# Performance work log

Measured on AMD Instinct MI355X. Metric: run time of the kernel, lower is better.

The kernel has to match this reference:

```python
import jax, jax.numpy as jnp
import numpy as np

N = 4096          # in_features
M = 4096          # out_features
RANK = 64
FT = 16           # ft_rank (trainable LoRA)
RES = RANK - FT   # frozen low-rank residual
CB = 65536        # E8P: 16-bit codeword per group of 8 weights
CW = 8            # codeword width (E8 lattice dim)
Q_SCALE = 0.02
GLOBAL_SCALE = 1.0


def _hadamard(n):
    # Sylvester construction, normalized: H @ H.T = I (matches matmul_hadU/hadUt up to transpose; H is symmetric)
    H = np.array([[1.0]], dtype=np.float32)
    while H.shape[0] < n:
        H = np.block([[H, H], [H, -H]])
    return H / np.sqrt(np.float32(n))


def setup_inputs() -> dict:
    key = jax.random.key(0)
    ks = jax.random.split(key, 9)
    x = jax.random.normal(ks[0], (8192, N), jnp.float32)
    Q_idxs = jax.random.randint(ks[1], (M, N // CW), 0, CB, dtype=jnp.int32)
    grid = jax.random.normal(ks[2], (CB, CW), jnp.float32) * 0.5   # E8P codebook grid
    SU = jax.random.rademacher(ks[3], (N,), dtype=jnp.float32)     # random sign vectors (QuIP#)
    SV = jax.random.rademacher(ks[4], (M,), dtype=jnp.float32)
    L_ft = jax.random.normal(ks[5], (M, FT), jnp.float32) * 0.02
    R_ft = jax.random.normal(ks[6], (FT, N), jnp.float32) * 0.02
    L_res = jax.random.normal(ks[7], (M, RES), jnp.float32) * 0.02
    R_res = jax.random.normal(ks[8], (RES, N), jnp.float32) * 0.02
    had_left = jnp.asarray(_hadamard(N))
    had_right = jnp.asarray(_hadamard(M))
    return {"x": x, "SU": SU, "SV": SV, "grid": grid, "L_ft": L_ft, "R_ft": R_ft,
            "L_res": L_res, "R_res": R_res, "had_left": had_left,
            "had_right": had_right, "Q_idxs": Q_idxs}


def reference(x, SU, SV, grid, L_ft, R_ft, L_res, R_res, had_left, had_right, Q_idxs):
    shape = x.shape
    h = x.reshape(-1, N) * SU                 # x * SU
    h = h @ had_left                          # matmul_hadUt (Hadamard is symmetric orthogonal)
    # E8P codebook decode: gather 8-dim codewords -> full [M, N] weight, fused matmul
    W = grid[Q_idxs].reshape(M, N)            # [M, N//8, 8] -> [M, N]
    out = (h @ W.T) * Q_SCALE                 # Q.forward
    out = out + (h @ R_res.T) @ L_res.T       # frozen low-rank residual (rank - ft_rank)
    out = out + (h @ R_ft.T) @ L_ft.T         # trainable LoRA path
    out = (out @ had_right) * GLOBAL_SCALE    # matmul_hadU * global_scale
    out = out * SV
    return out.reshape(*shape[:-1], M)
```

## Files before the change

kernel.cpp:

```cpp
#include <hip/hip_runtime.h>
#include <hip/hip_bf16.h>
#include <stdint.h>


typedef __bf16 bf16;
typedef __bf16 bf16x8 __attribute__((ext_vector_type(8)));
typedef float f32x4 __attribute__((ext_vector_type(4)));

#define KE 4160
#define NN 4096
#define MM 4096
#define BB 8192

__global__ void prep_kernel(const float* __restrict__ Lft, const float* __restrict__ Rft,
                            const float* __restrict__ Lres, const float* __restrict__ Rres,
                            bf16* __restrict__ Rcat, bf16* __restrict__ Wq) {
  int tid = blockIdx.x * 256 + threadIdx.x;
  if (tid < 64 * 4096) {
    int r = tid >> 12, n = tid & 4095;
    float v = (r < 48) ? Rres[r * 4096 + n] : Rft[(r - 48) * 4096 + n];
    Rcat[tid] = (bf16)v;
  } else {
    int t2 = tid - 64 * 4096;
    int m = t2 >> 6, r = t2 & 63;
    float v = (r < 48) ? Lres[m * 48 + r] : Lft[m * 16 + (r - 48)];
    Wq[(size_t)m * KE + 4096 + r] = (bf16)v;
  }
}

__global__ void decode_kernel(const int* __restrict__ qidx, const float* __restrict__ grid,
                              bf16* __restrict__ Wq) {
  int tid = blockIdx.x * 256 + threadIdx.x;
  int m = tid >> 9, g = tid & 511;
  uint32_t idx = (uint32_t)qidx[tid];
  const float4* gp = (const float4*)(grid + (size_t)idx * 8);
  float4 w0 = gp[0], w1 = gp[1];
  bf16x8 o;
  o[0] = (bf16)(w0.x * 0.02f); o[1] = (bf16)(w0.y * 0.02f);
  o[2] = (bf16)(w0.z * 0.02f); o[3] = (bf16)(w0.w * 0.02f);
  o[4] = (bf16)(w1.x * 0.02f); o[5] = (bf16)(w1.y * 0.02f);
  o[6] = (bf16)(w1.z * 0.02f); o[7] = (bf16)(w1.w * 0.02f);
  *(bf16x8*)(Wq + (size_t)m * KE + g * 8) = o;
}

#define SK(i) ((i) + ((i) >> 5))

__global__ void fwht_pre_kernel(const float* __restrict__ src,
                                bf16* __restrict__ dst,
                                const float* __restrict__ SU) {
  __shared__ float buf[4224];
  const int row = blockIdx.x, t = threadIdx.x;
  const float4* sp = (const float4*)(src + (size_t)row * NN + t * 16);
  const float4* su = (const float4*)(SU + t * 16);
  float v[16];
#pragma unroll
  for (int q = 0; q < 4; ++q) {
    float4 a = sp[q], s = su[q];
    v[q * 4 + 0] = a.x * s.x; v[q * 4 + 1] = a.y * s.y;
    v[q * 4 + 2] = a.z * s.z; v[q * 4 + 3] = a.w * s.w;
  }
#pragma unroll
  for (int s = 1; s < 16; s <<= 1) {
#pragma unroll
    for (int i = 0; i < 16; ++i) {
      if (!(i & s)) { float a = v[i], b = v[i + s]; v[i] = a + b; v[i + s] = a - b; }
    }
  }
#pragma unroll
  for (int i = 0; i < 16; ++i) buf[SK(t * 16 + i)] = v[i];
  for (int s = 16; s < 4096; s <<= 1) {
    __syncthreads();
#pragma unroll
    for (int j = 0; j < 8; ++j) {
      int p = t + j * 256;
      int i = ((p & ~(s - 1)) << 1) | (p & (s - 1));
      float a = buf[SK(i)], b = buf[SK(i + s)];
      buf[SK(i)] = a + b; buf[SK(i + s)] = a - b;
    }
  }
  __syncthreads();
  bf16x8 o0, o1;
#pragma unroll
  for (int i = 0; i < 8; ++i) {
    o0[i] = (bf16)(buf[SK(t * 16 + i)] * 0.015625f);
    o1[i] = (bf16)(buf[SK(t * 16 + 8 + i)] * 0.015625f);
  }
  bf16* dp = dst + (size_t)row * KE + t * 16;
  *(bf16x8*)dp = o0;
  *(bf16x8*)(dp + 8) = o1;
}

__global__ void fwht_post_kernel(float* __restrict__ data, const float* __restrict__ SV) {
  __shared__ float buf[4224];
  const int row = blockIdx.x, t = threadIdx.x;
  float4* dp = (float4*)(data + (size_t)row * MM + t * 16);
  float v[16];
#pragma unroll
  for (int q = 0; q < 4; ++q) {
    float4 a = dp[q];
    v[q * 4 + 0] = a.x; v[q * 4 + 1] = a.y; v[q * 4 + 2] = a.z; v[q * 4 + 3] = a.w;
  }
#pragma unroll
  for (int s = 1; s < 16; s <<= 1) {
#pragma unroll
    for (int i = 0; i < 16; ++i) {
      if (!(i & s)) { float a = v[i], b = v[i + s]; v[i] = a + b; v[i + s] = a - b; }
    }
  }
#pragma unroll
  for (int i = 0; i < 16; ++i) buf[SK(t * 16 + i)] = v[i];
  for (int s = 16; s < 4096; s <<= 1) {
    __syncthreads();
#pragma unroll
    for (int j = 0; j < 8; ++j) {
      int p = t + j * 256;
      int i = ((p & ~(s - 1)) << 1) | (p & (s - 1));
      float a = buf[SK(i)], b = buf[SK(i + s)];
      buf[SK(i)] = a + b; buf[SK(i + s)] = a - b;
    }
  }
  __syncthreads();
  const float4* sv = (const float4*)(SV + t * 16);
#pragma unroll
  for (int q = 0; q < 4; ++q) {
    float4 s = sv[q];
    float4 o;
    o.x = buf[SK(t * 16 + q * 4 + 0)] * 0.015625f * s.x;
    o.y = buf[SK(t * 16 + q * 4 + 1)] * 0.015625f * s.y;
    o.z = buf[SK(t * 16 + q * 4 + 2)] * 0.015625f * s.z;
    o.w = buf[SK(t * 16 + q * 4 + 3)] * 0.015625f * s.w;
    dp[q] = o;
  }
}

__global__ void __launch_bounds__(256) tgemm_kernel(const bf16* __restrict__ A,
                                                    const bf16* __restrict__ Bm,
                                                    float* __restrict__ Tpart) {
  __shared__ bf16 lA[128 * 32];
  __shared__ bf16 lB[64 * 32];
  const int t = threadIdx.x, w = t >> 6, l = t & 63;
  const int bmBlk = blockIdx.x;
  const int split = blockIdx.y;
  const int wm = w >> 1, wn = w & 1;
  f32x4 acc[4][2] = {};
  const int arow = t >> 1, acol = (t & 1) * 16;
  const bf16* pa = A + (size_t)(bmBlk * 128 + arow) * KE + acol;
  const int brow = (t & 127) >> 1, bcol = acol;
  const bf16* pb = Bm + (size_t)brow * 4096 + bcol;
  const int fr = l & 15, fk = (l >> 4) * 8;
  for (int kt = 0; kt < 32; ++kt) {
    const int k0 = (split * 32 + kt) * 32;
    bf16x8 a0 = *(const bf16x8*)(pa + k0);
    bf16x8 a1 = *(const bf16x8*)(pa + k0 + 8);
    *(bf16x8*)&lA[arow * 32 + acol] = a0;
    *(bf16x8*)&lA[arow * 32 + acol + 8] = a1;
    if (t < 128) {
      bf16x8 b0 = *(const bf16x8*)(pb + k0);
      bf16x8 b1 = *(const bf16x8*)(pb + k0 + 8);
      *(bf16x8*)&lB[brow * 32 + bcol] = b0;
      *(bf16x8*)&lB[brow * 32 + bcol + 8] = b1;
    }
    __syncthreads();
    bf16x8 af[4], bfr[2];
#pragma unroll
    for (int i = 0; i < 4; ++i) af[i] = *(const bf16x8*)&lA[(wm * 64 + i * 16 + fr) * 32 + fk];
#pragma unroll
    for (int i = 0; i < 2; ++i) bfr[i] = *(const bf16x8*)&lB[(wn * 32 + i * 16 + fr) * 32 + fk];
#pragma unroll
    for (int mi = 0; mi < 4; ++mi)
#pragma unroll
      for (int ni = 0; ni < 2; ++ni)
        acc[mi][ni] = __builtin_amdgcn_mfma_f32_16x16x32_bf16(af[mi], bfr[ni], acc[mi][ni], 0, 0, 0);
    __syncthreads();
  }
  float* out = Tpart + (size_t)split * BB * 64;
  const int orow = bmBlk * 128 + wm * 64 + (l >> 4) * 4;
  const int ocol = wn * 32 + (l & 15);
#pragma unroll
  for (int mi = 0; mi < 4; ++mi)
#pragma unroll
    for (int ni = 0; ni < 2; ++ni)
#pragma unroll
      for (int r = 0; r < 4; ++r)
        out[(size_t)(orow + mi * 16 + r) * 64 + ocol + ni * 16] = acc[mi][ni][r];
}

__global__ void tconv_kernel(const float* __restrict__ Tpart, bf16* __restrict__ h) {
  int i = blockIdx.x * 256 + threadIdx.x;
  float s = Tpart[i] + Tpart[i + BB * 64] + Tpart[i + 2 * BB * 64] + Tpart[i + 3 * BB * 64];
  int row = i >> 6, c = i & 63;
  h[(size_t)row * KE + 4096 + c] = (bf16)s;
}


__device__ __forceinline__ void gload16(const void* g, void* l) {
  __builtin_amdgcn_global_load_lds(
      (const __attribute__((address_space(1))) void*)g,
      (__attribute__((address_space(3))) void*)l, 16, 0, 0);
}

__device__ __forceinline__ void bar() {
  asm volatile("" ::: "memory");
  __builtin_amdgcn_s_barrier();
  asm volatile("" ::: "memory");
}

__global__ void __launch_bounds__(512, 2) mgemm_kernel(const bf16* __restrict__ A,
                                                       const bf16* __restrict__ B,
                                                       float* __restrict__ C) {
  __shared__ alignas(16) char sA[65536];
  __shared__ alignas(16) char sB[65536];
  const int t = threadIdx.x;
  const int w = t >> 6, l = t & 63;
  const int wm = w >> 2, wn = w & 3;
  const int bid = blockIdx.x;
  const int swzb = (bid & 7) * 64 + (bid >> 3);
  const int bm = swzb >> 4, bn = swzb & 15;

  const int c0 = w * 2, c1 = w * 2 + 1;
  const int lb0 = c0 * 1024 + l * 16;
  const int lb1 = c1 * 1024 + l * 16;
  const int sb0 = lb0 ^ (((lb0 >> 7) & 3) << 4);
  const int sb1 = lb1 ^ (((lb1 >> 7) & 3) << 4);
  const char* gA0 = (const char*)(A + (size_t)(bm * 256 + (sb0 >> 6)) * KE) + (sb0 & 63);
  const char* gA1 = (const char*)(A + (size_t)(bm * 256 + (sb1 >> 6)) * KE) + (sb1 & 63);
  const char* gB0 = (const char*)(B + (size_t)(bn * 256 + (sb0 >> 6)) * KE) + (sb0 & 63);
  const char* gB1 = (const char*)(B + (size_t)(bn * 256 + (sb1 >> 6)) * KE) + (sb1 & 63);

  const int fr = l & 15, fkb = (l >> 4) * 16;
  int offA[8], offB[4];
#pragma unroll
  for (int mi = 0; mi < 8; ++mi) {
    int lb = (wm * 128 + mi * 16 + fr) * 64 + fkb;
    offA[mi] = lb ^ (((lb >> 7) & 3) << 4);
  }
#pragma unroll
  for (int ni = 0; ni < 4; ++ni) {
    int lb = (wn * 64 + ni * 16 + fr) * 64 + fkb;
    offB[ni] = lb ^ (((lb >> 7) & 3) << 4);
  }

  f32x4 acc[8][4] = {};

#pragma unroll
  for (int p = 0; p < 3; ++p) {
    gload16(gA0 + (size_t)p * 64, &sA[p * 16384 + c0 * 1024]);
    gload16(gA1 + (size_t)p * 64, &sA[p * 16384 + c1 * 1024]);
    gload16(gB0 + (size_t)p * 64, &sB[p * 16384 + c0 * 1024]);
    gload16(gB1 + (size_t)p * 64, &sB[p * 16384 + c1 * 1024]);
  }
  asm volatile("s_waitcnt vmcnt(8)" ::: "memory");
  __builtin_amdgcn_sched_barrier(0);
  bar();

  for (int i = 0; i < 130; ++i) {
    const int sbs = (i & 3) << 14;
    const int s3b = ((i + 3) & 3) << 14;
    const size_t ko = (size_t)(i + 3) << 6;
    if (i < 127) {
      gload16(gA0 + ko, &sA[s3b + c0 * 1024]);
      gload16(gA1 + ko, &sA[s3b + c1 * 1024]);
      gload16(gB0 + ko, &sB[s3b + c0 * 1024]);
      gload16(gB1 + ko, &sB[s3b + c1 * 1024]);
    }
    bf16x8 af[8], bv[4];
#pragma unroll
    for (int ni = 0; ni < 4; ++ni) bv[ni] = *(const bf16x8*)&sB[sbs + offB[ni]];
#pragma unroll
    for (int mi = 0; mi < 8; ++mi) af[mi] = *(const bf16x8*)&sA[sbs + offA[mi]];
    __builtin_amdgcn_s_setprio(1);
#pragma unroll
    for (int mi = 0; mi < 8; ++mi)
#pragma unroll
      for (int ni = 0; ni < 4; ++ni)
        acc[mi][ni] = __builtin_amdgcn_mfma_f32_16x16x32_bf16(af[mi], bv[ni], acc[mi][ni], 0, 0, 0);
    __builtin_amdgcn_s_setprio(0);
    if (i < 127) {
      asm volatile("s_waitcnt vmcnt(8)" ::: "memory");
    } else if (i == 127) {
      asm volatile("s_waitcnt vmcnt(4)" ::: "memory");
    } else if (i == 128) {
      asm volatile("s_waitcnt vmcnt(0)" ::: "memory");
    }
    __builtin_amdgcn_sched_barrier(0);
    bar();
  }

  const int orow = bm * 256 + wm * 128 + ((l >> 4) << 2);
  const int ocol = bn * 256 + wn * 64 + (l & 15);
#pragma unroll
  for (int mi = 0; mi < 8; ++mi)
#pragma unroll
    for (int ni = 0; ni < 4; ++ni)
#pragma unroll
      for (int r = 0; r < 4; ++r)
        C[(size_t)(orow + mi * 16 + r) * MM + ocol + ni * 16] = acc[mi][ni][r];
}

extern "C" void kernel_launch(void* const* d_in, const int* in_sizes, int n_in,
                              void* d_out, int out_size, void* d_ws, size_t ws_size,
                              hipStream_t stream) {
  const float* x    = (const float*)d_in[0];
  const float* SU   = (const float*)d_in[1];
  const float* SV   = (const float*)d_in[2];
  const float* grid = (const float*)d_in[3];
  const float* Lft  = (const float*)d_in[4];
  const float* Rft  = (const float*)d_in[5];
  const float* Lres = (const float*)d_in[6];
  const float* Rres = (const float*)d_in[7];
  const int*   qidx = (const int*)d_in[10];
  float* out = (float*)d_out;

  char* ws = (char*)d_ws;
  bf16*  h     = (bf16*)ws;
  bf16*  Wq    = (bf16*)(ws + 68157440);
  bf16*  Rcat  = (bf16*)(ws + 68157440 + 34078720);
  float* Tpart = (float*)(ws + 68157440 + 34078720 + 524288);

  prep_kernel<<<2048, 256, 0, stream>>>(Lft, Rft, Lres, Rres, Rcat, Wq);
  decode_kernel<<<8192, 256, 0, stream>>>(qidx, grid, Wq);
  fwht_pre_kernel<<<8192, 256, 0, stream>>>(x, h, SU);
  tgemm_kernel<<<dim3(64, 4), 256, 0, stream>>>(h, Rcat, Tpart);
  tconv_kernel<<<2048, 256, 0, stream>>>(Tpart, h);
  mgemm_kernel<<<512, 512, 0, stream>>>(h, Wq, out);
  fwht_post_kernel<<<8192, 256, 0, stream>>>(out, SV);
}
```

Baseline: 714.4 us.

## Interleave GEMM LDS reads, global loads and MFMA in half-tile phases; drop FWHT padding

The main GEMM loop is unrolled by two K-steps and split into four phases. Each phase reads half the A fragments, issues part of the next global-to-LDS loads, hits a barrier, then runs 16 MFMAs, so memory traffic and compute interleave more finely, in the style of a ping-pong schedule. This adds many more barriers per iteration and changes the vmcnt wait accounting, which could stall or race if the counts are wrong. The FWHT kernels also drop the shared-memory padding swizzle, which may bring back LDS bank conflicts on the butterfly strides.

```diff
diff --git a/kernel.cpp b/kernel.cpp
--- a/kernel.cpp
+++ b/kernel.cpp
@@ -43,12 +43,10 @@
   *(bf16x8*)(Wq + (size_t)m * KE + g * 8) = o;
 }
 
-#define SK(i) ((i) + ((i) >> 5))
-
 __global__ void fwht_pre_kernel(const float* __restrict__ src,
                                 bf16* __restrict__ dst,
                                 const float* __restrict__ SU) {
-  __shared__ float buf[4224];
+  __shared__ float buf[4096];
   const int row = blockIdx.x, t = threadIdx.x;
   const float4* sp = (const float4*)(src + (size_t)row * NN + t * 16);
   const float4* su = (const float4*)(SU + t * 16);
@@ -67,23 +65,23 @@
     }
   }
 #pragma unroll
-  for (int i = 0; i < 16; ++i) buf[SK(t * 16 + i)] = v[i];
+  for (int i = 0; i < 16; ++i) buf[t * 16 + i] = v[i];
   for (int s = 16; s < 4096; s <<= 1) {
     __syncthreads();
 #pragma unroll
     for (int j = 0; j < 8; ++j) {
       int p = t + j * 256;
       int i = ((p & ~(s - 1)) << 1) | (p & (s - 1));
-      float a = buf[SK(i)], b = buf[SK(i + s)];
-      buf[SK(i)] = a + b; buf[SK(i + s)] = a - b;
+      float a = buf[i], b = buf[i + s];
+      buf[i] = a + b; buf[i + s] = a - b;
     }
   }
   __syncthreads();
   bf16x8 o0, o1;
 #pragma unroll
   for (int i = 0; i < 8; ++i) {
-    o0[i] = (bf16)(buf[SK(t * 16 + i)] * 0.015625f);
-    o1[i] = (bf16)(buf[SK(t * 16 + 8 + i)] * 0.015625f);
+    o0[i] = (bf16)(buf[t * 16 + i] * 0.015625f);
+    o1[i] = (bf16)(buf[t * 16 + 8 + i] * 0.015625f);
   }
   bf16* dp = dst + (size_t)row * KE + t * 16;
   *(bf16x8*)dp = o0;
@@ -91,7 +89,7 @@
 }
 
 __global__ void fwht_post_kernel(float* __restrict__ data, const float* __restrict__ SV) {
-  __shared__ float buf[4224];
+  __shared__ float buf[4096];
   const int row = blockIdx.x, t = threadIdx.x;
   float4* dp = (float4*)(data + (size_t)row * MM + t * 16);
   float v[16];
@@ -108,15 +106,15 @@
     }
   }
 #pragma unroll
-  for (int i = 0; i < 16; ++i) buf[SK(t * 16 + i)] = v[i];
+  for (int i = 0; i < 16; ++i) buf[t * 16 + i] = v[i];
   for (int s = 16; s < 4096; s <<= 1) {
     __syncthreads();
 #pragma unroll
     for (int j = 0; j < 8; ++j) {
       int p = t + j * 256;
       int i = ((p & ~(s - 1)) << 1) | (p & (s - 1));
-      float a = buf[SK(i)], b = buf[SK(i + s)];
-      buf[SK(i)] = a + b; buf[SK(i + s)] = a - b;
+      float a = buf[i], b = buf[i + s];
+      buf[i] = a + b; buf[i + s] = a - b;
     }
   }
   __syncthreads();
@@ -125,10 +123,10 @@
   for (int q = 0; q < 4; ++q) {
     float4 s = sv[q];
     float4 o;
-    o.x = buf[SK(t * 16 + q * 4 + 0)] * 0.015625f * s.x;
-    o.y = buf[SK(t * 16 + q * 4 + 1)] * 0.015625f * s.y;
-    o.z = buf[SK(t * 16 + q * 4 + 2)] * 0.015625f * s.z;
-    o.w = buf[SK(t * 16 + q * 4 + 3)] * 0.015625f * s.w;
+    o.x = buf[t * 16 + q * 4 + 0] * 0.015625f * s.x;
+    o.y = buf[t * 16 + q * 4 + 1] * 0.015625f * s.y;
+    o.z = buf[t * 16 + q * 4 + 2] * 0.015625f * s.z;
+    o.w = buf[t * 16 + q * 4 + 3] * 0.015625f * s.w;
     dp[q] = o;
   }
 }
@@ -205,6 +203,22 @@
   asm volatile("" ::: "memory");
 }
 
+#define RD_A(half, sbs) \
+  _Pragma("unroll") \
+  for (int mi = 0; mi < 4; ++mi) af[mi] = *(const bf16x8*)&sA[(sbs) + offA[(half) * 4 + mi]];
+#define RD_B(sbs) \
+  _Pragma("unroll") \
+  for (int ni = 0; ni < 4; ++ni) bv[ni] = *(const bf16x8*)&sB[(sbs) + offB[ni]];
+#define MFMA16(base) \
+  __builtin_amdgcn_s_setprio(1); \
+  _Pragma("unroll") \
+  for (int mi = 0; mi < 4; ++mi) \
+    _Pragma("unroll") \
+    for (int ni = 0; ni < 4; ++ni) \
+      acc[(base) + mi][ni] = \
+          __builtin_amdgcn_mfma_f32_16x16x32_bf16(af[mi], bv[ni], acc[(base) + mi][ni], 0, 0, 0); \
+  __builtin_amdgcn_s_setprio(0);
+
 __global__ void __launch_bounds__(512, 2) mgemm_kernel(const bf16* __restrict__ A,
                                                        const bf16* __restrict__ B,
                                                        float* __restrict__ C) {
@@ -243,46 +257,71 @@
   f32x4 acc[8][4] = {};
 
 #pragma unroll
-  for (int p = 0; p < 3; ++p) {
-    gload16(gA0 + (size_t)p * 64, &sA[p * 16384 + c0 * 1024]);
-    gload16(gA1 + (size_t)p * 64, &sA[p * 16384 + c1 * 1024]);
-    gload16(gB0 + (size_t)p * 64, &sB[p * 16384 + c0 * 1024]);
-    gload16(gB1 + (size_t)p * 64, &sB[p * 16384 + c1 * 1024]);
-  }
-  asm volatile("s_waitcnt vmcnt(8)" ::: "memory");
+  for (int k = 0; k < 3; ++k) {
+    gload16(gA0 + ((size_t)k << 6), &sA[(k << 14) + c0 * 1024]);
+    gload16(gA1 + ((size_t)k << 6), &sA[(k << 14) + c1 * 1024]);
+    gload16(gB0 + ((size_t)k << 6), &sB[(k << 14) + c0 * 1024]);
+    gload16(gB1 + ((size_t)k << 6), &sB[(k << 14) + c1 * 1024]);
+  }
+  asm volatile("s_waitcnt vmcnt(4)" ::: "memory");
   __builtin_amdgcn_sched_barrier(0);
   bar();
 
-  for (int i = 0; i < 130; ++i) {
-    const int sbs = (i & 3) << 14;
-    const int s3b = ((i + 3) & 3) << 14;
-    const size_t ko = (size_t)(i + 3) << 6;
-    if (i < 127) {
-      gload16(gA0 + ko, &sA[s3b + c0 * 1024]);
-      gload16(gA1 + ko, &sA[s3b + c1 * 1024]);
-      gload16(gB0 + ko, &sB[s3b + c0 * 1024]);
-      gload16(gB1 + ko, &sB[s3b + c1 * 1024]);
-    }
-    bf16x8 af[8], bv[4];
-#pragma unroll
-    for (int ni = 0; ni < 4; ++ni) bv[ni] = *(const bf16x8*)&sB[sbs + offB[ni]];
-#pragma unroll
-    for (int mi = 0; mi < 8; ++mi) af[mi] = *(const bf16x8*)&sA[sbs + offA[mi]];
-    __builtin_amdgcn_s_setprio(1);
-#pragma unroll
-    for (int mi = 0; mi < 8; ++mi)
-#pragma unroll
-      for (int ni = 0; ni < 4; ++ni)
-        acc[mi][ni] = __builtin_amdgcn_mfma_f32_16x16x32_bf16(af[mi], bv[ni], acc[mi][ni], 0, 0, 0);
-    __builtin_amdgcn_s_setprio(0);
-    if (i < 127) {
+  for (int j = 0; j < 65; ++j) {
+    const int sbs0 = (j & 1) << 15;
+    const int sbs1 = sbs0 + 16384;
+    const int k3 = 2 * j + 3, k4 = 2 * j + 4;
+    const size_t ko3 = (size_t)k3 << 6, ko4 = (size_t)k4 << 6;
+    const int sl3 = (k3 & 3) << 14, sl4 = (k4 & 3) << 14;
+    bf16x8 af[4], bv[4];
+
+    RD_A(0, sbs0)
+    RD_B(sbs0)
+    if (j <= 63) {
+      gload16(gA0 + ko3, &sA[sl3 + c0 * 1024]);
+      gload16(gA1 + ko3, &sA[sl3 + c1 * 1024]);
+    }
+    bar();
+    MFMA16(0)
+    bar();
+
+    RD_A(1, sbs0)
+    if (j <= 63) {
+      gload16(gB0 + ko3, &sB[sl3 + c0 * 1024]);
+      gload16(gB1 + ko3, &sB[sl3 + c1 * 1024]);
+    }
+    bar();
+    MFMA16(4)
+    if (j <= 63) {
       asm volatile("s_waitcnt vmcnt(8)" ::: "memory");
-    } else if (i == 127) {
-      asm volatile("s_waitcnt vmcnt(4)" ::: "memory");
-    } else if (i == 128) {
+      __builtin_amdgcn_sched_barrier(0);
+    }
+    bar();
+
+    RD_A(0, sbs1)
+    RD_B(sbs1)
+    if (j <= 62) {
+      gload16(gA0 + ko4, &sA[sl4 + c0 * 1024]);
+      gload16(gA1 + ko4, &sA[sl4 + c1 * 1024]);
+    }
+    bar();
+    MFMA16(0)
+    bar();
+
+    RD_A(1, sbs1)
+    if (j <= 62) {
+      gload16(gB0 + ko4, &sB[sl4 + c0 * 1024]);
+      gload16(gB1 + ko4, &sB[sl4 + c1 * 1024]);
+    }
+    bar();
+    MFMA16(4)
+    if (j <= 62) {
+      asm volatile("s_waitcnt vmcnt(8)" ::: "memory");
+      __builtin_amdgcn_sched_barrier(0);
+    } else if (j == 63) {
       asm volatile("s_waitcnt vmcnt(0)" ::: "memory");
-    }
-    __builtin_amdgcn_sched_barrier(0);
+      __builtin_amdgcn_sched_barrier(0);
+    }
     bar();
   }
 
```

New measurement: 688.8 us. 3.6% less time.
